# Optimization experiments

Measured on AMD Instinct MI355X. Metric: run time of the kernel, lower is better.

## Reference

```python
import jax, jax.numpy as jnp
import numpy as np

N, K, IN_C, OUT_C = 100000, 128, 128, 128


def setup_inputs() -> dict:
    key = jax.random.key(0)
    k1, k2, k3 = jax.random.split(key, 3)
    x = jax.random.normal(k1, (N, IN_C), dtype=jnp.float32)
    U = jax.random.normal(k2, (N, K), dtype=jnp.float32)
    coeffs = jax.random.normal(k3, (OUT_C, K, IN_C), dtype=jnp.float32)
    return {"x": x, "U": U, "coeffs": coeffs}


def reference(x, U, coeffs):
    # U.T @ x : (K, in_channels)
    spec = jnp.einsum('nk,ni->ki', U, x)
    # coeffs * spec, summed over in_channels : (out_channels, K)
    mixed = jnp.einsum('oki,ki->ok', coeffs, spec)
    # U @ mixed : (out_channels, N)
    out = jnp.einsum('nk,ok->on', U, mixed)
    # softmax over N (dim=-1), then transpose -> (N, out_channels)
    return jax.nn.softmax(out, axis=-1).T
```

## Files before the change

kernel.cpp:

```cpp
#include <hip/hip_runtime.h>
#include <math.h>

#define N_PTS 100000
#define KDIM 128
#define CDIM 128
#define TILE_N 64
#define NB1 ((N_PTS + TILE_N - 1) / TILE_N)

typedef short s16x8 __attribute__((ext_vector_type(8)));
typedef float f32x4 __attribute__((ext_vector_type(4)));

static __device__ __forceinline__ unsigned short f2bf(float f) {
    unsigned int u = __float_as_uint(f);
    unsigned int r = (u + 0x7FFFu + ((u >> 16) & 1u)) >> 16;
    return (unsigned short)r;
}
static __device__ __forceinline__ float bf2f(unsigned short h) {
    return __uint_as_float(((unsigned int)h) << 16);
}

static __device__ __forceinline__ void split_trunc(float v, unsigned short& hi, unsigned short& lo) {
    unsigned int u = __float_as_uint(v);
    unsigned int uh = u & 0xFFFF0000u;
    float lf = v - __uint_as_float(uh);
    hi = (unsigned short)(u >> 16);
    lo = (unsigned short)(__float_as_uint(lf) >> 16);
}

static __device__ __forceinline__ int frag_dst(int nloc, int c) {
    return (c >> 4) * 512 + (((nloc >> 3) & 3) * 16 + (c & 15)) * 8 + (nloc & 7);
}

__global__ __launch_bounds__(512, 4) void kA(const float* __restrict__ U,
                                             const float* __restrict__ x,
                                             float* __restrict__ partials,
                                             int chunk) {
    __shared__ unsigned short Ah_[8192], Al_[8192], Bh_[8192], Bl_[8192];
    const int tid = threadIdx.x;
    const int b = blockIdx.x;
    const int n_begin = b * chunk;
    const int n_end = min(N_PTS, n_begin + chunk);
    const int lane = tid & 63;
    const int w = tid >> 6;
    const int mtb = (w & 3) * 2;
    const int ntb = (w >> 2) * 4;
    const int quad = lane >> 4;
    const int nl = lane & 15;

    const int sc = tid & 127;
    const int rq = tid >> 7;

    f32x4 acc[2][4];
#pragma unroll
    for (int mi = 0; mi < 2; ++mi)
#pragma unroll
        for (int ni = 0; ni < 4; ++ni) acc[mi][ni] = (f32x4)(0.0f);

    for (int n0 = n_begin; n0 < n_end; n0 += 64) {
#pragma unroll
        for (int p = 0; p < 2; ++p) {
            const int nb = rq * 16 + p * 8;
            float uv[8], xv[8];
#pragma unroll
            for (int jj = 0; jj < 8; ++jj) {
                int gn = n0 + nb + jj;
                bool ok = (gn < n_end);
                uv[jj] = ok ? U[(size_t)gn * 128 + sc] : 0.0f;
                xv[jj] = ok ? x[(size_t)gn * 128 + sc] : 0.0f;
            }
            s16x8 uh, ul, xh, xl;
#pragma unroll
            for (int jj = 0; jj < 8; ++jj) {
                unsigned short h, l;
                split_trunc(uv[jj], h, l);
                uh[jj] = (short)h; ul[jj] = (short)l;
                split_trunc(xv[jj], h, l);
                xh[jj] = (short)h; xl[jj] = (short)l;
            }
            const int sub = nb >> 5;
            const int dst = sub * 4096 + frag_dst(nb & 31, sc);
            *(s16x8*)&Ah_[dst] = uh;
            *(s16x8*)&Al_[dst] = ul;
            *(s16x8*)&Bh_[dst] = xh;
            *(s16x8*)&Bl_[dst] = xl;
        }
        __syncthreads();

#pragma unroll
        for (int sub = 0; sub < 2; ++sub) {
            const int base = sub * 4096;
            s16x8 ah[2], al[2];
#pragma unroll
            for (int mi = 0; mi < 2; ++mi) {
                ah[mi] = *(s16x8*)&Ah_[base + (mtb + mi) * 512 + lane * 8];
                al[mi] = *(s16x8*)&Al_[base + (mtb + mi) * 512 + lane * 8];
            }
#pragma unroll
            for (int ni = 0; ni < 4; ++ni) {
                s16x8 bh = *(s16x8*)&Bh_[base + (ntb + ni) * 512 + lane * 8];
                s16x8 bl = *(s16x8*)&Bl_[base + (ntb + ni) * 512 + lane * 8];
#pragma unroll
                for (int mi = 0; mi < 2; ++mi) {
                    acc[mi][ni] = __builtin_amdgcn_mfma_f32_16x16x32_bf16(ah[mi], bh, acc[mi][ni], 0, 0, 0);
                    acc[mi][ni] = __builtin_amdgcn_mfma_f32_16x16x32_bf16(al[mi], bh, acc[mi][ni], 0, 0, 0);
                    acc[mi][ni] = __builtin_amdgcn_mfma_f32_16x16x32_bf16(ah[mi], bl, acc[mi][ni], 0, 0, 0);
                }
            }
        }
        __syncthreads();
    }

    float* p = partials + (size_t)b * 16384;
#pragma unroll
    for (int mi = 0; mi < 2; ++mi) {
#pragma unroll
        for (int reg = 0; reg < 4; ++reg) {
            int k = (mtb + mi) * 16 + quad * 4 + reg;
#pragma unroll
            for (int ni = 0; ni < 4; ++ni) {
                int i = (ntb + ni) * 16 + nl;
                p[k * 128 + i] = acc[mi][ni][reg];
            }
        }
    }
}

__global__ __launch_bounds__(256) void kA2a(const float* __restrict__ partials,
                                            float* __restrict__ partial2, int nA) {
    const int jc = blockIdx.x >> 3;
    const int s = blockIdx.x & 7;
    const int j = jc * 256 + threadIdx.x;
    const int per = (nA + 7) >> 3;
    int b = s * per;
    const int be = min(b + per, nA);
    float a0 = 0.0f, a1 = 0.0f, a2 = 0.0f, a3 = 0.0f;
    for (; b + 4 <= be; b += 4) {
        a0 += partials[(size_t)(b + 0) * 16384 + j];
        a1 += partials[(size_t)(b + 1) * 16384 + j];
        a2 += partials[(size_t)(b + 2) * 16384 + j];
        a3 += partials[(size_t)(b + 3) * 16384 + j];
    }
    for (; b < be; ++b) a0 += partials[(size_t)b * 16384 + j];
    partial2[(size_t)s * 16384 + j] = (a0 + a1) + (a2 + a3);
}

__global__ __launch_bounds__(256) void kA2b(const float* __restrict__ partial2,
                                            float* __restrict__ spec) {
    int j = blockIdx.x * 256 + threadIdx.x;
    float v0 = partial2[j];
    float v1 = partial2[16384 + j];
    float v2 = partial2[2 * 16384 + j];
    float v3 = partial2[3 * 16384 + j];
    float v4 = partial2[4 * 16384 + j];
    float v5 = partial2[5 * 16384 + j];
    float v6 = partial2[6 * 16384 + j];
    float v7 = partial2[7 * 16384 + j];
    spec[j] = ((v0 + v1) + (v2 + v3)) + ((v4 + v5) + (v6 + v7));
}

__global__ __launch_bounds__(256) void kB(const float* __restrict__ coeffs,
                                          const float* __restrict__ spec,
                                          unsigned short* __restrict__ afrag_hi,
                                          unsigned short* __restrict__ afrag_lo) {
    int wave = (blockIdx.x * 256 + threadIdx.x) >> 6;
    int lane = threadIdx.x & 63;
    int o = wave >> 7;
    int k = wave & 127;
    float2 c2 = *(const float2*)&coeffs[((size_t)o * 128 + k) * 128 + lane * 2];
    float2 s2 = *(const float2*)&spec[k * 128 + lane * 2];
    float v = c2.x * s2.x + c2.y * s2.y;
#pragma unroll
    for (int s = 32; s >= 1; s >>= 1) v += __shfl_xor(v, s);
    if (lane == 0) {
        unsigned short hi = f2bf(v);
        unsigned short lo = f2bf(v - bf2f(hi));
        int idx = ((o >> 4) * 4 + (k >> 5)) * 512 + (((k >> 3) & 3) * 16 + (o & 15)) * 8 + (k & 7);
        afrag_hi[idx] = hi;
        afrag_lo[idx] = lo;
    }
}

__global__ __launch_bounds__(512) void kC1(const float* __restrict__ U,
                                           const unsigned short* __restrict__ afrag_hi,
                                           const unsigned short* __restrict__ afrag_lo,
                                           float* __restrict__ out,
                                           float* __restrict__ m_part,
                                           float* __restrict__ l_part) {
    __shared__ unsigned short Bh[8192];
    __shared__ unsigned short Bl[8192];
    const int tid = threadIdx.x;
    const int b = blockIdx.x;
    const int n0 = b * TILE_N;
    const int lane = tid & 63;
    const int w = tid >> 6;
    const int quad = lane >> 4;
    const int nl = lane & 15;

#pragma unroll
    for (int r = 0; r < 4; ++r) {
        int idx = (r * 512 + tid) * 4;
        int n = idx >> 7;
        int k = idx & 127;
        int gn = n0 + n;
        float4 u4 = (gn < N_PTS) ? *(const float4*)&U[(size_t)gn * 128 + k]
                                 : make_float4(0, 0, 0, 0);
        unsigned short h0 = f2bf(u4.x), h1 = f2bf(u4.y), h2 = f2bf(u4.z), h3 = f2bf(u4.w);
        unsigned short l0 = f2bf(u4.x - bf2f(h0));
        unsigned short l1 = f2bf(u4.y - bf2f(h1));
        unsigned short l2 = f2bf(u4.z - bf2f(h2));
        unsigned short l3 = f2bf(u4.w - bf2f(h3));
        int dst = ((k >> 5) * 4 + (n >> 4)) * 512 + (((k >> 3) & 3) * 16 + (n & 15)) * 8 + (k & 7);
        uint2 hp, lp;
        hp.x = (unsigned int)h0 | ((unsigned int)h1 << 16);
        hp.y = (unsigned int)h2 | ((unsigned int)h3 << 16);
        lp.x = (unsigned int)l0 | ((unsigned int)l1 << 16);
        lp.y = (unsigned int)l2 | ((unsigned int)l3 << 16);
        *(uint2*)&Bh[dst] = hp;
        *(uint2*)&Bl[dst] = lp;
    }

    s16x8 Ah[4], Al[4];
#pragma unroll
    for (int kc = 0; kc < 4; ++kc) {
        size_t aoff = (size_t)(w * 4 + kc) * 512 + lane * 8;
        Ah[kc] = *(const s16x8*)(afrag_hi + aoff);
        Al[kc] = *(const s16x8*)(afrag_lo + aoff);
    }

    __syncthreads();

    f32x4 acc[4];
#pragma unroll
    for (int nt = 0; nt < 4; ++nt) acc[nt] = (f32x4)(0.0f);

#pragma unroll
    for (int kc = 0; kc < 4; ++kc) {
#pragma unroll
        for (int nt = 0; nt < 4; ++nt) {
            int boff = ((kc * 4 + nt) * 512) + lane * 8;
            s16x8 bh = *(s16x8*)&Bh[boff];
            s16x8 bl = *(s16x8*)&Bl[boff];
            acc[nt] = __builtin_amdgcn_mfma_f32_16x16x32_bf16(Ah[kc], bh, acc[nt], 0, 0, 0);
            acc[nt] = __builtin_amdgcn_mfma_f32_16x16x32_bf16(Al[kc], bh, acc[nt], 0, 0, 0);
            acc[nt] = __builtin_amdgcn_mfma_f32_16x16x32_bf16(Ah[kc], bl, acc[nt], 0, 0, 0);
        }
    }

#pragma unroll
    for (int nt = 0; nt < 4; ++nt) {
        if (n0 + nt * 16 + nl >= N_PTS) {
#pragma unroll
            for (int reg = 0; reg < 4; ++reg) acc[nt][reg] = -3.4e38f;
        }
    }

    float mb[4];
#pragma unroll
    for (int reg = 0; reg < 4; ++reg)
        mb[reg] = fmaxf(fmaxf(acc[0][reg], acc[1][reg]), fmaxf(acc[2][reg], acc[3][reg]));
#pragma unroll
    for (int s = 1; s < 16; s <<= 1) {
#pragma unroll
        for (int reg = 0; reg < 4; ++reg) mb[reg] = fmaxf(mb[reg], __shfl_xor(mb[reg], s));
    }

#pragma unroll
    for (int nt = 0; nt < 4; ++nt) {
#pragma unroll
        for (int reg = 0; reg < 4; ++reg) acc[nt][reg] = __expf(acc[nt][reg] - mb[reg]);
        int gn = n0 + nt * 16 + nl;
        if (gn < N_PTS)
            *(f32x4*)&out[(size_t)gn * 128 + w * 16 + quad * 4] = acc[nt];
    }

    float ls[4];
#pragma unroll
    for (int reg = 0; reg < 4; ++reg)
        ls[reg] = ((acc[0][reg] + acc[1][reg]) + (acc[2][reg] + acc[3][reg]));
#pragma unroll
    for (int s = 1; s < 16; s <<= 1) {
#pragma unroll
        for (int reg = 0; reg < 4; ++reg) ls[reg] += __shfl_xor(ls[reg], s);
    }

    if (nl == 0) {
#pragma unroll
        for (int reg = 0; reg < 4; ++reg) {
            int o = w * 16 + quad * 4 + reg;
            m_part[(size_t)o * NB1 + b] = mb[reg];
            l_part[(size_t)o * NB1 + b] = ls[reg];
        }
    }
}

__global__ __launch_bounds__(256) void kC2(const float* __restrict__ m_part,
                                           const float* __restrict__ l_part,
                                           float* __restrict__ scale) {
    const int o = blockIdx.x;
    const int tid = threadIdx.x;
    const float* __restrict__ mp = m_part + (size_t)o * NB1;
    const float* __restrict__ lp = l_part + (size_t)o * NB1;
    __shared__ float sm[256];
    float m = -3.4e38f;
    for (int b = tid; b < NB1; b += 256) m = fmaxf(m, mp[b]);
    sm[tid] = m;
    __syncthreads();
    for (int s = 128; s >= 1; s >>= 1) {
        if (tid < s) sm[tid] = fmaxf(sm[tid], sm[tid + s]);
        __syncthreads();
    }
    m = sm[0];
    __syncthreads();
    float l = 0.0f;
    for (int b = tid; b < NB1; b += 256)
        l += lp[b] * __expf(mp[b] - m);
    sm[tid] = l;
    __syncthreads();
    for (int s = 128; s >= 1; s >>= 1) {
        if (tid < s) sm[tid] += sm[tid + s];
        __syncthreads();
    }
    l = sm[0];
    float inv = 1.0f / l;
    for (int b = tid; b < NB1; b += 256)
        scale[(size_t)o * NB1 + b] = __expf(mp[b] - m) * inv;
}

__global__ __launch_bounds__(256) void kC3(float* __restrict__ out,
                                           const float* __restrict__ scale) {
    const int b = blockIdx.x;
    const int tid = threadIdx.x;
    __shared__ float sc[128];
    if (tid < 128) sc[tid] = scale[(size_t)tid * NB1 + b];
    __syncthreads();
    const int n0 = b * TILE_N;
#pragma unroll
    for (int r = 0; r < 8; ++r) {
        int idx = (r * 256 + tid) * 4;
        int n = idx >> 7;
        int o = idx & 127;
        int gn = n0 + n;
        if (gn < N_PTS) {
            float4 v = *(float4*)&out[(size_t)gn * 128 + o];
            v.x *= sc[o];
            v.y *= sc[o + 1];
            v.z *= sc[o + 2];
            v.w *= sc[o + 3];
            *(float4*)&out[(size_t)gn * 128 + o] = v;
        }
    }
}

extern "C" void kernel_launch(void* const* d_in, const int* in_sizes, int n_in,
                              void* d_out, int out_size, void* d_ws, size_t ws_size,
                              hipStream_t stream) {
    const float* x = (const float*)d_in[0];
    const float* U = (const float*)d_in[1];
    const float* coeffs = (const float*)d_in[2];
    float* out = (float*)d_out;

    float* f = (float*)d_ws;
    float* spec = f;
    unsigned short* afrag_hi = (unsigned short*)(f + 16384);
    unsigned short* afrag_lo = (unsigned short*)(f + 16384 + 8192);
    float* m_part = f + 16384 + 16384;
    float* l_part = m_part + (size_t)128 * NB1;
    float* scale = l_part + (size_t)128 * NB1;
    float* partial2 = scale + (size_t)128 * NB1;
    float* partialsA = partial2 + 8 * 16384;

    size_t fixed_bytes = ((size_t)(16384 * 2) + (size_t)NB1 * 128 * 3 + (size_t)8 * 16384) * 4;
    int nA = 512;
    if (ws_size > fixed_bytes) {
        size_t avail = (ws_size - fixed_bytes) / 65536;
        if ((size_t)nA > avail) nA = (int)avail;
    } else {
        nA = 1;
    }
    if (nA < 1) nA = 1;
    int chunk = (N_PTS + nA - 1) / nA;

    kA<<<nA, 512, 0, stream>>>(U, x, partialsA, chunk);
    kA2a<<<512, 256, 0, stream>>>(partialsA, partial2, nA);
    kA2b<<<64, 256, 0, stream>>>(partial2, spec);
    kB<<<4096, 256, 0, stream>>>(coeffs, spec, afrag_hi, afrag_lo);
    kC1<<<NB1, 512, 0, stream>>>(U, afrag_hi, afrag_lo, out, m_part, l_part);
    kC2<<<128, 256, 0, stream>>>(m_part, l_part, scale);
    kC3<<<NB1, 256, 0, stream>>>(out, scale);
}
```

Before: 206.5 us.

## Vectorize staging loads with XOR-swizzled LDS layout and fuse spec reduction into kB

In kA, each thread now loads float4 rows from one of U or x (split across half the block) instead of scalar loads of both. The shared-memory fragment layout is XOR-swizzled to cut LDS bank conflicts on both the writes and the MFMA operand reads. kC1's U staging is rewritten the same way, writing 8-element swizzled vectors, and it switches from round-to-nearest bf16 splitting to truncation splitting. The kA2b reduction kernel is removed and its 8-way sum is folded into kB, saving one launch at the cost of redundant partial2 reads across output channels.

```diff
diff --git a/kernel.cpp b/kernel.cpp
--- a/kernel.cpp
+++ b/kernel.cpp
@@ -27,15 +27,12 @@
     lo = (unsigned short)(__float_as_uint(lf) >> 16);
 }
 
-static __device__ __forceinline__ int frag_dst(int nloc, int c) {
-    return (c >> 4) * 512 + (((nloc >> 3) & 3) * 16 + (c & 15)) * 8 + (nloc & 7);
-}
-
 __global__ __launch_bounds__(512, 4) void kA(const float* __restrict__ U,
                                              const float* __restrict__ x,
                                              float* __restrict__ partials,
                                              int chunk) {
-    __shared__ unsigned short Ah_[8192], Al_[8192], Bh_[8192], Bl_[8192];
+    __shared__ unsigned short Hs[2][8192];
+    __shared__ unsigned short Ls[2][8192];
     const int tid = threadIdx.x;
     const int b = blockIdx.x;
     const int n_begin = b * chunk;
@@ -47,8 +44,13 @@
     const int quad = lane >> 4;
     const int nl = lane & 15;
 
-    const int sc = tid & 127;
-    const int rq = tid >> 7;
+    const int arr = tid >> 8;
+    const float* __restrict__ src = arr ? x : U;
+    const int c4 = (tid & 31) * 4;
+    const int rq = (tid >> 5) & 7;
+    const int Tt = c4 >> 4;
+    const int ssub = rq >> 2;
+    const int R = rq & 3;
 
     f32x4 acc[2][4];
 #pragma unroll
@@ -57,32 +59,28 @@
         for (int ni = 0; ni < 4; ++ni) acc[mi][ni] = (f32x4)(0.0f);
 
     for (int n0 = n_begin; n0 < n_end; n0 += 64) {
-#pragma unroll
-        for (int p = 0; p < 2; ++p) {
-            const int nb = rq * 16 + p * 8;
-            float uv[8], xv[8];
-#pragma unroll
-            for (int jj = 0; jj < 8; ++jj) {
-                int gn = n0 + nb + jj;
-                bool ok = (gn < n_end);
-                uv[jj] = ok ? U[(size_t)gn * 128 + sc] : 0.0f;
-                xv[jj] = ok ? x[(size_t)gn * 128 + sc] : 0.0f;
-            }
-            s16x8 uh, ul, xh, xl;
+        float4 v[8];
+#pragma unroll
+        for (int jj = 0; jj < 8; ++jj) {
+            int gn = n0 + rq * 8 + jj;
+            v[jj] = (gn < n_end) ? *(const float4*)&src[(size_t)gn * 128 + c4]
+                                 : make_float4(0, 0, 0, 0);
+        }
+#pragma unroll
+        for (int cc = 0; cc < 4; ++cc) {
+            s16x8 hh, ll;
 #pragma unroll
             for (int jj = 0; jj < 8; ++jj) {
                 unsigned short h, l;
-                split_trunc(uv[jj], h, l);
-                uh[jj] = (short)h; ul[jj] = (short)l;
-                split_trunc(xv[jj], h, l);
-                xh[jj] = (short)h; xl[jj] = (short)l;
-            }
-            const int sub = nb >> 5;
-            const int dst = sub * 4096 + frag_dst(nb & 31, sc);
-            *(s16x8*)&Ah_[dst] = uh;
-            *(s16x8*)&Al_[dst] = ul;
-            *(s16x8*)&Bh_[dst] = xh;
-            *(s16x8*)&Bl_[dst] = xl;
+                split_trunc(((const float*)&v[jj])[cc], h, l);
+                hh[jj] = (short)h;
+                ll[jj] = (short)l;
+            }
+            const int c = c4 + cc;
+            const int g = Tt * 64 + R * 16 + ((c & 15) ^ Tt);
+            const int dst = ssub * 4096 + g * 8;
+            *(s16x8*)&Hs[arr][dst] = hh;
+            *(s16x8*)&Ls[arr][dst] = ll;
         }
         __syncthreads();
 
@@ -92,13 +90,17 @@
             s16x8 ah[2], al[2];
 #pragma unroll
             for (int mi = 0; mi < 2; ++mi) {
-                ah[mi] = *(s16x8*)&Ah_[base + (mtb + mi) * 512 + lane * 8];
-                al[mi] = *(s16x8*)&Al_[base + (mtb + mi) * 512 + lane * 8];
+                const int T = mtb + mi;
+                const int off = base + (T * 64 + quad * 16 + (nl ^ T)) * 8;
+                ah[mi] = *(s16x8*)&Hs[0][off];
+                al[mi] = *(s16x8*)&Ls[0][off];
             }
 #pragma unroll
             for (int ni = 0; ni < 4; ++ni) {
-                s16x8 bh = *(s16x8*)&Bh_[base + (ntb + ni) * 512 + lane * 8];
-                s16x8 bl = *(s16x8*)&Bl_[base + (ntb + ni) * 512 + lane * 8];
+                const int T2 = ntb + ni;
+                const int off = base + (T2 * 64 + quad * 16 + (nl ^ T2)) * 8;
+                s16x8 bh = *(s16x8*)&Hs[1][off];
+                s16x8 bl = *(s16x8*)&Ls[1][off];
 #pragma unroll
                 for (int mi = 0; mi < 2; ++mi) {
                     acc[mi][ni] = __builtin_amdgcn_mfma_f32_16x16x32_bf16(ah[mi], bh, acc[mi][ni], 0, 0, 0);
@@ -144,31 +146,27 @@
     partial2[(size_t)s * 16384 + j] = (a0 + a1) + (a2 + a3);
 }
 
-__global__ __launch_bounds__(256) void kA2b(const float* __restrict__ partial2,
-                                            float* __restrict__ spec) {
-    int j = blockIdx.x * 256 + threadIdx.x;
-    float v0 = partial2[j];
-    float v1 = partial2[16384 + j];
-    float v2 = partial2[2 * 16384 + j];
-    float v3 = partial2[3 * 16384 + j];
-    float v4 = partial2[4 * 16384 + j];
-    float v5 = partial2[5 * 16384 + j];
-    float v6 = partial2[6 * 16384 + j];
-    float v7 = partial2[7 * 16384 + j];
-    spec[j] = ((v0 + v1) + (v2 + v3)) + ((v4 + v5) + (v6 + v7));
-}
-
 __global__ __launch_bounds__(256) void kB(const float* __restrict__ coeffs,
-                                          const float* __restrict__ spec,
+                                          const float* __restrict__ partial2,
                                           unsigned short* __restrict__ afrag_hi,
                                           unsigned short* __restrict__ afrag_lo) {
     int wave = (blockIdx.x * 256 + threadIdx.x) >> 6;
     int lane = threadIdx.x & 63;
     int o = wave >> 7;
     int k = wave & 127;
+    const int j = k * 128 + lane * 2;
+    float2 p0 = *(const float2*)&partial2[j];
+    float2 p1 = *(const float2*)&partial2[16384 + j];
+    float2 p2 = *(const float2*)&partial2[2 * 16384 + j];
+    float2 p3 = *(const float2*)&partial2[3 * 16384 + j];
+    float2 p4 = *(const float2*)&partial2[4 * 16384 + j];
+    float2 p5 = *(const float2*)&partial2[5 * 16384 + j];
+    float2 p6 = *(const float2*)&partial2[6 * 16384 + j];
+    float2 p7 = *(const float2*)&partial2[7 * 16384 + j];
+    float sx = ((p0.x + p1.x) + (p2.x + p3.x)) + ((p4.x + p5.x) + (p6.x + p7.x));
+    float sy = ((p0.y + p1.y) + (p2.y + p3.y)) + ((p4.y + p5.y) + (p6.y + p7.y));
     float2 c2 = *(const float2*)&coeffs[((size_t)o * 128 + k) * 128 + lane * 2];
-    float2 s2 = *(const float2*)&spec[k * 128 + lane * 2];
-    float v = c2.x * s2.x + c2.y * s2.y;
+    float v = c2.x * sx + c2.y * sy;
 #pragma unroll
     for (int s = 32; s >= 1; s >>= 1) v += __shfl_xor(v, s);
     if (lane == 0) {
@@ -196,27 +194,32 @@
     const int quad = lane >> 4;
     const int nl = lane & 15;
 
-#pragma unroll
-    for (int r = 0; r < 4; ++r) {
-        int idx = (r * 512 + tid) * 4;
-        int n = idx >> 7;
-        int k = idx & 127;
-        int gn = n0 + n;
-        float4 u4 = (gn < N_PTS) ? *(const float4*)&U[(size_t)gn * 128 + k]
-                                 : make_float4(0, 0, 0, 0);
-        unsigned short h0 = f2bf(u4.x), h1 = f2bf(u4.y), h2 = f2bf(u4.z), h3 = f2bf(u4.w);
-        unsigned short l0 = f2bf(u4.x - bf2f(h0));
-        unsigned short l1 = f2bf(u4.y - bf2f(h1));
-        unsigned short l2 = f2bf(u4.z - bf2f(h2));
-        unsigned short l3 = f2bf(u4.w - bf2f(h3));
-        int dst = ((k >> 5) * 4 + (n >> 4)) * 512 + (((k >> 3) & 3) * 16 + (n & 15)) * 8 + (k & 7);
-        uint2 hp, lp;
-        hp.x = (unsigned int)h0 | ((unsigned int)h1 << 16);
-        hp.y = (unsigned int)h2 | ((unsigned int)h3 << 16);
-        lp.x = (unsigned int)l0 | ((unsigned int)l1 << 16);
-        lp.y = (unsigned int)l2 | ((unsigned int)l3 << 16);
-        *(uint2*)&Bh[dst] = hp;
-        *(uint2*)&Bl[dst] = lp;
+    {
+        const int sn = tid & 63;
+        const int k8b = tid >> 6;
+        const int gn = n0 + sn;
+#pragma unroll
+        for (int r = 0; r < 2; ++r) {
+            const int k0 = (k8b + r * 8) * 8;
+            float4 f0 = make_float4(0, 0, 0, 0), f1 = make_float4(0, 0, 0, 0);
+            if (gn < N_PTS) {
+                f0 = *(const float4*)&U[(size_t)gn * 128 + k0];
+                f1 = *(const float4*)&U[(size_t)gn * 128 + k0 + 4];
+            }
+            float vv[8] = {f0.x, f0.y, f0.z, f0.w, f1.x, f1.y, f1.z, f1.w};
+            s16x8 hh, ll;
+#pragma unroll
+            for (int jj = 0; jj < 8; ++jj) {
+                unsigned short h, l;
+                split_trunc(vv[jj], h, l);
+                hh[jj] = (short)h;
+                ll[jj] = (short)l;
+            }
+            const int T = (k0 >> 5) * 4 + (sn >> 4);
+            const int g = T * 64 + ((k0 >> 3) & 3) * 16 + ((sn & 15) ^ (T & 3));
+            *(s16x8*)&Bh[g * 8] = hh;
+            *(s16x8*)&Bl[g * 8] = ll;
+        }
     }
 
     s16x8 Ah[4], Al[4];
@@ -237,9 +240,10 @@
     for (int kc = 0; kc < 4; ++kc) {
 #pragma unroll
         for (int nt = 0; nt < 4; ++nt) {
-            int boff = ((kc * 4 + nt) * 512) + lane * 8;
-            s16x8 bh = *(s16x8*)&Bh[boff];
-            s16x8 bl = *(s16x8*)&Bl[boff];
+            const int T = kc * 4 + nt;
+            const int g = T * 64 + quad * 16 + (nl ^ (T & 3));
+            s16x8 bh = *(s16x8*)&Bh[g * 8];
+            s16x8 bl = *(s16x8*)&Bl[g * 8];
             acc[nt] = __builtin_amdgcn_mfma_f32_16x16x32_bf16(Ah[kc], bh, acc[nt], 0, 0, 0);
             acc[nt] = __builtin_amdgcn_mfma_f32_16x16x32_bf16(Al[kc], bh, acc[nt], 0, 0, 0);
             acc[nt] = __builtin_amdgcn_mfma_f32_16x16x32_bf16(Ah[kc], bl, acc[nt], 0, 0, 0);
@@ -368,6 +372,7 @@
     float* scale = l_part + (size_t)128 * NB1;
     float* partial2 = scale + (size_t)128 * NB1;
     float* partialsA = partial2 + 8 * 16384;
+    (void)spec;
 
     size_t fixed_bytes = ((size_t)(16384 * 2) + (size_t)NB1 * 128 * 3 + (size_t)8 * 16384) * 4;
     int nA = 512;
@@ -382,8 +387,7 @@
 
     kA<<<nA, 512, 0, stream>>>(U, x, partialsA, chunk);
     kA2a<<<512, 256, 0, stream>>>(partialsA, partial2, nA);
-    kA2b<<<64, 256, 0, stream>>>(partial2, spec);
-    kB<<<4096, 256, 0, stream>>>(coeffs, spec, afrag_hi, afrag_lo);
+    kB<<<4096, 256, 0, stream>>>(coeffs, partial2, afrag_hi, afrag_lo);
     kC1<<<NB1, 512, 0, stream>>>(U, afrag_hi, afrag_lo, out, m_part, l_part);
     kC2<<<128, 256, 0, stream>>>(m_part, l_part, scale);
     kC3<<<NB1, 256, 0, stream>>>(out, scale);
```

Result: slower. 212.0 us (+2.7%).
